# Optimization experiments

Hardware: AMD Instinct MI355X
Metric: run time of the kernel (lower is better)

Reference implementation:

```python
import jax, jax.numpy as jnp
import numpy as np

K_MAX = 3
ITERS = 3
NEG_BIG = -1e9


def squash(x):
    # x: [..., O]
    sn = jnp.sum(jnp.square(x), axis=-1, keepdims=True)
    factor = sn / (1.0 + sn) / jnp.sqrt(sn + 1e-8)
    return factor * x


def setup_inputs() -> dict:
    key = jax.random.key(0)
    k1, k2, k3, k4 = jax.random.split(key, 4)
    N, L, D, O = 4096, 200, 64, 64
    behavior_embs = jax.random.normal(k1, (N, L, D), dtype=jnp.float32)
    W = jax.random.normal(k2, (D, O), dtype=jnp.float32)  # init_std=1.0
    routing_logits_init = jax.random.normal(k3, (N, K_MAX, L), dtype=jnp.float32)
    seq_len = jax.random.randint(k4, (N, 1), 0, L, dtype=jnp.int32)
    return {
        "behavior_embs": behavior_embs,
        "W": W,
        "routing_logits_init": routing_logits_init,
        "seq_len": seq_len,
    }


def reference(behavior_embs, W, routing_logits_init, seq_len):
    N, L, D = behavior_embs.shape
    # mask: [N, K_MAX, L] -- valid positions along L, tiled across capsules
    mask = jnp.arange(L)[None, None, :] < seq_len[:, None, :]  # [N,1,L]
    mask = jnp.broadcast_to(mask, (N, K_MAX, L))

    mappings = jnp.matmul(behavior_embs, W)          # [N, L, O]
    m_det = jax.lax.stop_gradient(mappings)         # routing uses detached mappings

    logits = routing_logits_init                     # [N, K_MAX, L]
    for _ in range(ITERS - 1):
        padded = jnp.where(mask, logits, NEG_BIG)
        # NOTE: softmax over the capsule dim (axis=1), as in the original
        weights = jax.nn.softmax(padded, axis=1)     # [N, K_MAX, L]
        candidates = jnp.matmul(weights, m_det)      # [N, K_MAX, O]
        interests = squash(candidates)
        logits = logits + jnp.einsum('nko,nlo->nkl', interests, m_det)

    padded = jnp.where(mask, logits, NEG_BIG)
    weights = jax.nn.softmax(padded, axis=1)
    candidates = jnp.matmul(weights, mappings)       # final iter uses non-detached
    interests = squash(candidates)                   # [N, K_MAX, O]
    return interests
```

## Files before the change

### kernel.cpp

```cpp
#include <hip/hip_runtime.h>
#include <math.h>

typedef _Float16 f16;
typedef _Float16 f16x8 __attribute__((ext_vector_type(8)));
typedef float f32x4 __attribute__((ext_vector_type(4)));

#define LSEQ 200
#define LT 13
#define LKS 7

__global__ __launch_bounds__(256, 2)
void capsule_kernel(const float* __restrict__ E,
                    const float* __restrict__ W,
                    const float* __restrict__ RL,
                    const int* __restrict__ SL,
                    float* __restrict__ out)
{
    __shared__ f16 E_sw[LT*2*64*8];
    __shared__ f16 W_sw[4*2*64*8];
    __shared__ f16 mT_sw[4*LKS*64*8];
    __shared__ f16 w_sw[LKS*64*8];
    __shared__ f16 i_sw[2*64*8];
    __shared__ float logits[3*LSEQ];
    __shared__ float cand[3*64];

    const int n = blockIdx.x;
    const int t = threadIdx.x;
    const int lane = t & 63;
    const int wv = t >> 6;

    const float4 f4z = make_float4(0.f, 0.f, 0.f, 0.f);
    for (int g = t; g < 448;  g += 256) *(float4*)&w_sw[g*8]  = f4z;
    for (int g = t; g < 128;  g += 256) *(float4*)&i_sw[g*8]  = f4z;
    for (int g = t; g < 1792; g += 256) *(float4*)&mT_sw[g*8] = f4z;

    const float* Eb = E + (size_t)n * (LSEQ*64);
    for (int g = t; g < LT*2*64; g += 256) {
        int sb = g >> 6, c = g & 63;
        int Tl = sb >> 1, ks = sb & 1;
        int q = c >> 4, m = c & 15;
        int l = Tl*16 + m;
        int kb = ks*32 + q*8;
        float4 v0 = f4z, v1 = f4z;
        if (l < LSEQ) {
            v0 = *(const float4*)(Eb + l*64 + kb);
            v1 = *(const float4*)(Eb + l*64 + kb + 4);
        }
        f16x8 h = { (f16)v0.x,(f16)v0.y,(f16)v0.z,(f16)v0.w,
                    (f16)v1.x,(f16)v1.y,(f16)v1.z,(f16)v1.w };
        *(f16x8*)&E_sw[g*8] = h;
    }

    for (int g = t; g < 512; g += 256) {
        int sb = g >> 6, c = g & 63;
        int To = sb >> 1, ks = sb & 1;
        int q = c >> 4, m = c & 15;
        int o = To*16 + m;
        int d0 = ks*32 + q*8;
        f16x8 h;
        #pragma unroll
        for (int j = 0; j < 8; j++) h[j] = (f16)W[(d0 + j)*64 + o];
        *(f16x8*)&W_sw[g*8] = h;
    }

    if (t < LSEQ) {
        const float* R = RL + (size_t)n * (3*LSEQ);
        logits[t]          = R[t];
        logits[LSEQ + t]   = R[LSEQ + t];
        logits[2*LSEQ + t] = R[2*LSEQ + t];
    }
    const int s = SL[n];

    __syncthreads();

    f32x4 acc[LT];
    {
        const int To = wv;
        #pragma unroll
        for (int Tl = 0; Tl < LT; Tl++) {
            f32x4 c0 = {0.f, 0.f, 0.f, 0.f};
            #pragma unroll
            for (int ks = 0; ks < 2; ks++) {
                f16x8 a = *(f16x8*)&E_sw[((Tl*2 + ks)*64 + lane)*8];
                f16x8 b = *(f16x8*)&W_sw[((To*2 + ks)*64 + lane)*8];
                c0 = __builtin_amdgcn_mfma_f32_16x16x32_f16(a, b, c0, 0, 0, 0);
            }
            acc[Tl] = c0;
        }
    }
    __syncthreads();

    {
        const int To = wv;
        const int q4 = lane >> 4, cc = lane & 15;
        const int o = To*16 + cc;
        const int kso = o >> 5, qo = (o & 31) >> 3, jo = o & 7;
        #pragma unroll
        for (int Tl = 0; Tl < LT; Tl++) {
            #pragma unroll
            for (int r = 0; r < 4; r++) {
                f16 h = (f16)acc[Tl][r];
                int lp = q4*4 + r;
                int l  = Tl*16 + lp;
                E_sw [((Tl*2 + kso)*64 + qo*16 + lp)*8 + jo] = h;
                mT_sw[((To*LKS + (l >> 5))*64 + ((l & 31) >> 3)*16 + cc)*8 + (lp & 7)] = h;
            }
        }
    }
    __syncthreads();

    for (int iter = 0; iter < 3; iter++) {
        if (t < LSEQ) {
            float w0, w1, w2;
            if (t < s) {
                float l0 = logits[t], l1 = logits[LSEQ + t], l2 = logits[2*LSEQ + t];
                float mx = fmaxf(fmaxf(l0, l1), l2);
                float e0 = expf(l0 - mx), e1 = expf(l1 - mx), e2 = expf(l2 - mx);
                float inv = 1.f / (e0 + e1 + e2);
                w0 = e0*inv; w1 = e1*inv; w2 = e2*inv;
            } else {
                w0 = w1 = w2 = (1.f/3.f);
            }
            int ks = t >> 5, q = (t & 31) >> 3, j = t & 7;
            int base = (ks*64 + q*16)*8 + j;
            w_sw[base]      = (f16)w0;
            w_sw[base + 8]  = (f16)w1;
            w_sw[base + 16] = (f16)w2;
        }
        __syncthreads();

        f32x4 ca = {0.f, 0.f, 0.f, 0.f};
        #pragma unroll
        for (int ks = 0; ks < LKS; ks++) {
            f16x8 a = *(f16x8*)&w_sw[(ks*64 + lane)*8];
            f16x8 b = *(f16x8*)&mT_sw[((wv*LKS + ks)*64 + lane)*8];
            ca = __builtin_amdgcn_mfma_f32_16x16x32_f16(a, b, ca, 0, 0, 0);
        }
        if (lane < 16) {
            #pragma unroll
            for (int r = 0; r < 3; r++) cand[r*64 + wv*16 + lane] = ca[r];
        }
        __syncthreads();

        if (t < 192) {
            float x = cand[t];
            float sq = x*x;
            #pragma unroll
            for (int off = 32; off >= 1; off >>= 1) sq += __shfl_xor(sq, off, 64);
            float factor = sq / ((1.f + sq) * sqrtf(sq + 1e-8f));
            float y = factor * x;
            if (iter < 2) {
                int k = t >> 6, o = t & 63;
                i_sw[(((o >> 5)*4 + ((o & 31) >> 3))*16 + k)*8 + (o & 7)] = (f16)y;
            } else {
                out[(size_t)n*192 + t] = y;
            }
        }
        if (iter == 2) break;
        __syncthreads();

        for (int Tn = wv; Tn < LT; Tn += 4) {
            f32x4 da = {0.f, 0.f, 0.f, 0.f};
            #pragma unroll
            for (int kso = 0; kso < 2; kso++) {
                f16x8 a = *(f16x8*)&i_sw[(kso*64 + lane)*8];
                f16x8 b = *(f16x8*)&E_sw[((Tn*2 + kso)*64 + lane)*8];
                da = __builtin_amdgcn_mfma_f32_16x16x32_f16(a, b, da, 0, 0, 0);
            }
            if (lane < 16) {
                int l = Tn*16 + lane;
                if (l < LSEQ) {
                    logits[l]          += da[0];
                    logits[LSEQ + l]   += da[1];
                    logits[2*LSEQ + l] += da[2];
                }
            }
        }
        __syncthreads();
    }
}

extern "C" void kernel_launch(void* const* d_in, const int* in_sizes, int n_in,
                              void* d_out, int out_size, void* d_ws, size_t ws_size,
                              hipStream_t stream) {
    const float* E  = (const float*)d_in[0];
    const float* W  = (const float*)d_in[1];
    const float* RL = (const float*)d_in[2];
    const int*   SL = (const int*)d_in[3];
    float* o = (float*)d_out;
    const int N = in_sizes[3];
    capsule_kernel<<<dim3(N), dim3(256), 0, stream>>>(E, W, RL, SL, o);
}
```

Before: 349.5 us.

## Keep W and mapping fragments in registers to cut LDS and raise occupancy

Each thread now loads its W columns straight from global memory into registers, so the W shared buffer is gone. The transposed mapping buffer is also removed: each wave gathers its candidate-matmul operand fragments once into registers and reuses them across all routing iterations, swapping the MFMA operand roles so the output layout changes. Launch bounds go from 2 to 4 blocks per CU, which the smaller LDS footprint allows. The cost is higher register pressure from the held fragments, a scattered per-element LDS gather, and uncoalesced global reads of W.

```diff
diff --git a/kernel.cpp b/kernel.cpp
--- a/kernel.cpp
+++ b/kernel.cpp
@@ -9,16 +9,14 @@
 #define LT 13
 #define LKS 7
 
-__global__ __launch_bounds__(256, 2)
+__global__ __launch_bounds__(256, 4)
 void capsule_kernel(const float* __restrict__ E,
                     const float* __restrict__ W,
                     const float* __restrict__ RL,
                     const int* __restrict__ SL,
                     float* __restrict__ out)
 {
-    __shared__ f16 E_sw[LT*2*64*8];
-    __shared__ f16 W_sw[4*2*64*8];
-    __shared__ f16 mT_sw[4*LKS*64*8];
+    __shared__ f16 m_sw[LT*2*64*8];
     __shared__ f16 w_sw[LKS*64*8];
     __shared__ f16 i_sw[2*64*8];
     __shared__ float logits[3*LSEQ];
@@ -28,19 +26,28 @@
     const int t = threadIdx.x;
     const int lane = t & 63;
     const int wv = t >> 6;
+    const int q = lane >> 4;
+    const int cc = lane & 15;
+
+    const int o_own = wv*16 + cc;
+    float wf[16];
+    #pragma unroll
+    for (int ks = 0; ks < 2; ks++)
+        #pragma unroll
+        for (int j = 0; j < 8; j++)
+            wf[ks*8 + j] = W[(ks*32 + q*8 + j)*64 + o_own];
 
     const float4 f4z = make_float4(0.f, 0.f, 0.f, 0.f);
-    for (int g = t; g < 448;  g += 256) *(float4*)&w_sw[g*8]  = f4z;
-    for (int g = t; g < 128;  g += 256) *(float4*)&i_sw[g*8]  = f4z;
-    for (int g = t; g < 1792; g += 256) *(float4*)&mT_sw[g*8] = f4z;
+    for (int g = t; g < 448; g += 256) *(float4*)&w_sw[g*8] = f4z;
+    for (int g = t; g < 128; g += 256) *(float4*)&i_sw[g*8] = f4z;
 
     const float* Eb = E + (size_t)n * (LSEQ*64);
     for (int g = t; g < LT*2*64; g += 256) {
         int sb = g >> 6, c = g & 63;
         int Tl = sb >> 1, ks = sb & 1;
-        int q = c >> 4, m = c & 15;
+        int qq = c >> 4, m = c & 15;
         int l = Tl*16 + m;
-        int kb = ks*32 + q*8;
+        int kb = ks*32 + qq*8;
         float4 v0 = f4z, v1 = f4z;
         if (l < LSEQ) {
             v0 = *(const float4*)(Eb + l*64 + kb);
@@ -48,19 +55,7 @@
         }
         f16x8 h = { (f16)v0.x,(f16)v0.y,(f16)v0.z,(f16)v0.w,
                     (f16)v1.x,(f16)v1.y,(f16)v1.z,(f16)v1.w };
-        *(f16x8*)&E_sw[g*8] = h;
-    }
-
-    for (int g = t; g < 512; g += 256) {
-        int sb = g >> 6, c = g & 63;
-        int To = sb >> 1, ks = sb & 1;
-        int q = c >> 4, m = c & 15;
-        int o = To*16 + m;
-        int d0 = ks*32 + q*8;
-        f16x8 h;
-        #pragma unroll
-        for (int j = 0; j < 8; j++) h[j] = (f16)W[(d0 + j)*64 + o];
-        *(f16x8*)&W_sw[g*8] = h;
+        *(f16x8*)&m_sw[g*8] = h;
     }
 
     if (t < LSEQ) {
@@ -73,41 +68,54 @@
 
     __syncthreads();
 
+    f16x8 wB[2];
+    #pragma unroll
+    for (int ks = 0; ks < 2; ks++) {
+        f16x8 h;
+        #pragma unroll
+        for (int j = 0; j < 8; j++) h[j] = (f16)wf[ks*8 + j];
+        wB[ks] = h;
+    }
     f32x4 acc[LT];
-    {
-        const int To = wv;
-        #pragma unroll
-        for (int Tl = 0; Tl < LT; Tl++) {
-            f32x4 c0 = {0.f, 0.f, 0.f, 0.f};
-            #pragma unroll
-            for (int ks = 0; ks < 2; ks++) {
-                f16x8 a = *(f16x8*)&E_sw[((Tl*2 + ks)*64 + lane)*8];
-                f16x8 b = *(f16x8*)&W_sw[((To*2 + ks)*64 + lane)*8];
-                c0 = __builtin_amdgcn_mfma_f32_16x16x32_f16(a, b, c0, 0, 0, 0);
-            }
-            acc[Tl] = c0;
-        }
+    #pragma unroll
+    for (int Tl = 0; Tl < LT; Tl++) {
+        f32x4 c0 = {0.f, 0.f, 0.f, 0.f};
+        #pragma unroll
+        for (int ks = 0; ks < 2; ks++) {
+            f16x8 a = *(f16x8*)&m_sw[((Tl*2 + ks)*64 + lane)*8];
+            c0 = __builtin_amdgcn_mfma_f32_16x16x32_f16(a, wB[ks], c0, 0, 0, 0);
+        }
+        acc[Tl] = c0;
     }
     __syncthreads();
 
-    {
-        const int To = wv;
-        const int q4 = lane >> 4, cc = lane & 15;
-        const int o = To*16 + cc;
-        const int kso = o >> 5, qo = (o & 31) >> 3, jo = o & 7;
-        #pragma unroll
-        for (int Tl = 0; Tl < LT; Tl++) {
-            #pragma unroll
-            for (int r = 0; r < 4; r++) {
-                f16 h = (f16)acc[Tl][r];
-                int lp = q4*4 + r;
-                int l  = Tl*16 + lp;
-                E_sw [((Tl*2 + kso)*64 + qo*16 + lp)*8 + jo] = h;
-                mT_sw[((To*LKS + (l >> 5))*64 + ((l & 31) >> 3)*16 + cc)*8 + (lp & 7)] = h;
-            }
+    const int kso = o_own >> 5, qo = (o_own & 31) >> 3, jo = o_own & 7;
+    #pragma unroll
+    for (int Tl = 0; Tl < LT; Tl++) {
+        #pragma unroll
+        for (int r = 0; r < 4; r++) {
+            int lp = q*4 + r;
+            m_sw[((Tl*2 + kso)*64 + qo*16 + lp)*8 + jo] = (f16)acc[Tl][r];
         }
     }
     __syncthreads();
+
+    f16x8 mfrag[LKS];
+    #pragma unroll
+    for (int ks = 0; ks < LKS; ks++) {
+        f16x8 h;
+        #pragma unroll
+        for (int j = 0; j < 8; j++) {
+            int l = ks*32 + q*8 + j;
+            f16 v = (f16)0.f;
+            if (l < 208) {
+                int Tl = l >> 4, lp = l & 15;
+                v = m_sw[((Tl*2 + kso)*64 + qo*16 + lp)*8 + jo];
+            }
+            h[j] = v;
+        }
+        mfrag[ks] = h;
+    }
 
     for (int iter = 0; iter < 3; iter++) {
         if (t < LSEQ) {
@@ -121,8 +129,8 @@
             } else {
                 w0 = w1 = w2 = (1.f/3.f);
             }
-            int ks = t >> 5, q = (t & 31) >> 3, j = t & 7;
-            int base = (ks*64 + q*16)*8 + j;
+            int ks = t >> 5, qq = (t & 31) >> 3, j = t & 7;
+            int base = (ks*64 + qq*16)*8 + j;
             w_sw[base]      = (f16)w0;
             w_sw[base + 8]  = (f16)w1;
             w_sw[base + 16] = (f16)w2;
@@ -132,13 +140,12 @@
         f32x4 ca = {0.f, 0.f, 0.f, 0.f};
         #pragma unroll
         for (int ks = 0; ks < LKS; ks++) {
-            f16x8 a = *(f16x8*)&w_sw[(ks*64 + lane)*8];
-            f16x8 b = *(f16x8*)&mT_sw[((wv*LKS + ks)*64 + lane)*8];
-            ca = __builtin_amdgcn_mfma_f32_16x16x32_f16(a, b, ca, 0, 0, 0);
-        }
-        if (lane < 16) {
+            f16x8 b = *(f16x8*)&w_sw[(ks*64 + lane)*8];
+            ca = __builtin_amdgcn_mfma_f32_16x16x32_f16(mfrag[ks], b, ca, 0, 0, 0);
+        }
+        if (cc < 3) {
             #pragma unroll
-            for (int r = 0; r < 3; r++) cand[r*64 + wv*16 + lane] = ca[r];
+            for (int r = 0; r < 4; r++) cand[cc*64 + wv*16 + q*4 + r] = ca[r];
         }
         __syncthreads();
 
@@ -162,9 +169,9 @@
         for (int Tn = wv; Tn < LT; Tn += 4) {
             f32x4 da = {0.f, 0.f, 0.f, 0.f};
             #pragma unroll
-            for (int kso = 0; kso < 2; kso++) {
-                f16x8 a = *(f16x8*)&i_sw[(kso*64 + lane)*8];
-                f16x8 b = *(f16x8*)&E_sw[((Tn*2 + kso)*64 + lane)*8];
+            for (int ko = 0; ko < 2; ko++) {
+                f16x8 a = *(f16x8*)&i_sw[(ko*64 + lane)*8];
+                f16x8 b = *(f16x8*)&m_sw[((Tn*2 + ko)*64 + lane)*8];
                 da = __builtin_amdgcn_mfma_f32_16x16x32_f16(a, b, da, 0, 0, 0);
             }
             if (lane < 16) {
```

New measurement: 313.4 us. 10.3% less time.
